# Kernel optimization log

Hardware: AMD Instinct MI355X
Metric: run time of the kernel (lower is better)

## Reference

```python
import jax, jax.numpy as jnp
import numpy as np

VOCAB_SIZE = 95
EMBED_DIM = 48
HIDDEN_DIM = 48


def setup_inputs() -> dict:
    key = jax.random.key(0)
    ks = jax.random.split(key, 8)
    B, S = 2048, 512
    x = jax.random.randint(ks[0], (B, S), 0, VOCAB_SIZE)
    s_e = 1.0  # torch Embedding default init ~ N(0,1); scale irrelevant for correctness
    emb = jax.random.normal(ks[1], (VOCAB_SIZE, EMBED_DIM), dtype=jnp.float32) * s_e
    k = 1.0 / np.sqrt(HIDDEN_DIM)
    w_ih = jax.random.uniform(ks[2], (3 * HIDDEN_DIM, EMBED_DIM), minval=-k, maxval=k, dtype=jnp.float32)
    w_hh = jax.random.uniform(ks[3], (3 * HIDDEN_DIM, HIDDEN_DIM), minval=-k, maxval=k, dtype=jnp.float32)
    b_ih = jax.random.uniform(ks[4], (3 * HIDDEN_DIM,), minval=-k, maxval=k, dtype=jnp.float32)
    b_hh = jax.random.uniform(ks[5], (3 * HIDDEN_DIM,), minval=-k, maxval=k, dtype=jnp.float32)
    w_out = jax.random.uniform(ks[6], (VOCAB_SIZE, HIDDEN_DIM), minval=-k, maxval=k, dtype=jnp.float32)
    b_out = jax.random.uniform(ks[7], (VOCAB_SIZE,), minval=-k, maxval=k, dtype=jnp.float32)
    return {"x": x, "emb": emb, "w_ih": w_ih, "w_hh": w_hh,
            "b_ih": b_ih, "b_hh": b_hh, "w_out": w_out, "b_out": b_out}


def _gru(embed, w_ih, w_hh, b_ih, b_hh):
    # embed: [B, S, E]. PyTorch GRU (single layer, batch_first):
    #   r = sig(Wir x + bir + Whr h + bhr); z = sig(Wiz x + biz + Whz h + bhz)
    B = embed.shape[0]
    H = w_hh.shape[1]
    # precompute input contributions for all timesteps: [S, B, 3H]
    xg = jnp.einsum('bse,ge->bsg', embed, w_ih) + b_ih
    xg = jnp.swapaxes(xg, 0, 1)
    h0 = jnp.zeros((B, H), dtype=embed.dtype)

    def step(h, xg_t):
        gh = h @ w_hh.T + b_hh  # [B, 3H]
        xr, xz, xn = jnp.split(xg_t, 3, axis=-1)
        hr, hz, hn = jnp.split(gh, 3, axis=-1)
        r = jax.nn.sigmoid(xr + hr)
        z = jax.nn.sigmoid(xz + hz)
        n = jnp.tanh(xn + r * hn)
        h_new = (1.0 - z) * n + z * h
        return h_new, h_new

    h_last, hs = jax.lax.scan(step, h0, xg)
    out = jnp.swapaxes(hs, 0, 1)  # [B, S, H]
    return out, h_last


def reference(x, emb, w_ih, w_hh, b_ih, b_hh, w_out, b_out):
    embed = emb[x]  # [B, S, E]
    out, h_last = _gru(embed, w_ih, w_hh, b_ih, b_hh)
    logits = jnp.einsum('bsh,vh->bsv', out, w_out) + b_out  # [B, S, V]
    hidden = h_last[None]  # [1, B, H] to match torch GRU hidden layout
    return logits, hidden
```

## Files before the change

### kernel.cpp

```cpp
#include <hip/hip_runtime.h>
#include <hip/hip_bf16.h>


#define BATCH 2048
#define SEQ   512
#define HDIM  48
#define VOCAB 95
#define G3    144

__device__ __forceinline__ float sigmoidf_(float x) {
    return 1.0f / (1.0f + __expf(-x));
}

__global__ void xg_precompute(const float* __restrict__ emb,
                              const float* __restrict__ w_ih,
                              const float* __restrict__ b_ih,
                              float* __restrict__ xg) {
    int v = blockIdx.x;
    int g = threadIdx.x;
    const float* e = emb + v * HDIM;
    const float* w = w_ih + g * HDIM;
    float a0 = 0.f, a1 = 0.f, a2 = 0.f, a3 = 0.f;
    #pragma unroll
    for (int k = 0; k < HDIM; k += 4) {
        a0 = fmaf(w[k + 0], e[k + 0], a0);
        a1 = fmaf(w[k + 1], e[k + 1], a1);
        a2 = fmaf(w[k + 2], e[k + 2], a2);
        a3 = fmaf(w[k + 3], e[k + 3], a3);
    }
    xg[v * G3 + g] = b_ih[g] + ((a0 + a1) + (a2 + a3));
}

__global__ __launch_bounds__(64, 2)
void gru_rec(const int* __restrict__ x,
             const float* __restrict__ xg_table,
             const float* __restrict__ w_hh,
             const float* __restrict__ b_hh,
             float* __restrict__ out,
             float* __restrict__ hidden) {
    const int row = blockIdx.x;
    const int j   = threadIdx.x;
    __shared__ float hsh[HDIM];

    float4 wr[12], wz[12], wn[12];
    float br = 0.f, bz = 0.f, bn = 0.f;
    float hj = 0.f;
    if (j < HDIM) {
        const float4* whr = (const float4*)(w_hh + (j         ) * HDIM);
        const float4* whz = (const float4*)(w_hh + (j +   HDIM) * HDIM);
        const float4* whn = (const float4*)(w_hh + (j + 2*HDIM) * HDIM);
        #pragma unroll
        for (int k = 0; k < 12; ++k) { wr[k] = whr[k]; wz[k] = whz[k]; wn[k] = whn[k]; }
        br = b_hh[j]; bz = b_hh[j + HDIM]; bn = b_hh[j + 2*HDIM];
        hsh[j] = 0.f;
    }
    __syncthreads();

    const int* xrow = x + row * SEQ;
    int tok = xrow[0];
    for (int t = 0; t < SEQ; ++t) {
        int tok_next = (t + 1 < SEQ) ? xrow[t + 1] : 0;
        float hnew = 0.f;
        if (j < HDIM) {
            const float* xg = xg_table + tok * G3;
            float xr = xg[j], xz = xg[j + HDIM], xn = xg[j + 2*HDIM];
            float accr = br, accz = bz, accn = bn;
            const float4* h4 = (const float4*)hsh;
            #pragma unroll
            for (int k = 0; k < 12; ++k) {
                float4 hh = h4[k];
                accr = fmaf(wr[k].x, hh.x, accr); accr = fmaf(wr[k].y, hh.y, accr);
                accr = fmaf(wr[k].z, hh.z, accr); accr = fmaf(wr[k].w, hh.w, accr);
                accz = fmaf(wz[k].x, hh.x, accz); accz = fmaf(wz[k].y, hh.y, accz);
                accz = fmaf(wz[k].z, hh.z, accz); accz = fmaf(wz[k].w, hh.w, accz);
                accn = fmaf(wn[k].x, hh.x, accn); accn = fmaf(wn[k].y, hh.y, accn);
                accn = fmaf(wn[k].z, hh.z, accn); accn = fmaf(wn[k].w, hh.w, accn);
            }
            float r = sigmoidf_(xr + accr);
            float z = sigmoidf_(xz + accz);
            float n = tanhf(xn + r * accn);
            hnew = (1.0f - z) * n + z * hj;
            hj = hnew;
            out[((long)(row * SEQ + t)) * VOCAB + j] = hnew;
        }
        __syncthreads();
        if (j < HDIM) hsh[j] = hnew;
        __syncthreads();
        tok = tok_next;
    }
    if (j < HDIM) hidden[row * HDIM + j] = hj;
}

__global__ __launch_bounds__(256, 2)
void logits_k(const float* __restrict__ w_out,
              const float* __restrict__ b_out,
              float* __restrict__ out) {
    __shared__ float hsh[256 * HDIM];
    const long pos0 = (long)blockIdx.x * 256;
    const int tid = threadIdx.x;

    for (int i = tid; i < 256 * HDIM; i += 256) {
        int p = i / HDIM;
        int k = i - p * HDIM;
        hsh[i] = out[(pos0 + p) * VOCAB + k];
    }
    __syncthreads();

    float h[HDIM];
    #pragma unroll
    for (int k = 0; k < 12; ++k)
        ((float4*)h)[k] = ((const float4*)(hsh + tid * HDIM))[k];

    float* orow = out + (pos0 + tid) * VOCAB;
    for (int v = 0; v < VOCAB; ++v) {
        const float* w = w_out + v * HDIM;
        float a0 = 0.f, a1 = 0.f, a2 = 0.f, a3 = 0.f;
        #pragma unroll
        for (int k = 0; k < HDIM; k += 4) {
            a0 = fmaf(w[k + 0], h[k + 0], a0);
            a1 = fmaf(w[k + 1], h[k + 1], a1);
            a2 = fmaf(w[k + 2], h[k + 2], a2);
            a3 = fmaf(w[k + 3], h[k + 3], a3);
        }
        orow[v] = b_out[v] + ((a0 + a1) + (a2 + a3));
    }
}

extern "C" void kernel_launch(void* const* d_in, const int* in_sizes, int n_in,
                              void* d_out, int out_size, void* d_ws, size_t ws_size,
                              hipStream_t stream) {
    const int*   x     = (const int*)d_in[0];
    const float* emb   = (const float*)d_in[1];
    const float* w_ih  = (const float*)d_in[2];
    const float* w_hh  = (const float*)d_in[3];
    const float* b_ih  = (const float*)d_in[4];
    const float* b_hh  = (const float*)d_in[5];
    const float* w_out = (const float*)d_in[6];
    const float* b_out = (const float*)d_in[7];

    float* out    = (float*)d_out;
    float* hidden = out + (long)BATCH * SEQ * VOCAB;
    float* xg     = (float*)d_ws;

    xg_precompute<<<VOCAB, G3, 0, stream>>>(emb, w_ih, b_ih, xg);
    gru_rec<<<BATCH, 64, 0, stream>>>(x, xg, w_hh, b_hh, out, hidden);
    logits_k<<<(BATCH * SEQ) / 256, 256, 0, stream>>>(w_out, b_out, out);
}
```

Measured before the change: 1.321 ms.

## Restructure logits kernel: split vocab across waves and stage output through LDS

The logits kernel now handles 64 positions per block, with each of the four waves computing a 24-wide slice of the vocabulary for the same 64 positions. Results go into shared memory and are then written back with coalesced float4 stores, replacing strided per-thread row writes of 95 floats. Hidden states are read with a padded stride of 49 to avoid LDS bank conflicts. This targets uncoalesced global stores in a kernel whose output dominates traffic, at the cost of extra LDS round trips and more blocks.

```diff
diff --git a/kernel.cpp b/kernel.cpp
--- a/kernel.cpp
+++ b/kernel.cpp
@@ -7,6 +7,7 @@
 #define HDIM  48
 #define VOCAB 95
 #define G3    144
+#define LPOS  64
 
 __device__ __forceinline__ float sigmoidf_(float x) {
     return 1.0f / (1.0f + __expf(-x));
@@ -91,28 +92,33 @@
     if (j < HDIM) hidden[row * HDIM + j] = hj;
 }
 
-__global__ __launch_bounds__(256, 2)
+__global__ __launch_bounds__(256, 4)
 void logits_k(const float* __restrict__ w_out,
               const float* __restrict__ b_out,
               float* __restrict__ out) {
-    __shared__ float hsh[256 * HDIM];
-    const long pos0 = (long)blockIdx.x * 256;
-    const int tid = threadIdx.x;
+    __shared__ __align__(16) float lsm[LPOS * VOCAB];
 
-    for (int i = tid; i < 256 * HDIM; i += 256) {
+    const long pos0 = (long)blockIdx.x * LPOS;
+    const int  tid  = threadIdx.x;
+    const int  lane = tid & 63;
+    const int  wv   = __builtin_amdgcn_readfirstlane(tid >> 6);
+
+    for (int i = tid; i < LPOS * HDIM; i += 256) {
         int p = i / HDIM;
         int k = i - p * HDIM;
-        hsh[i] = out[(pos0 + p) * VOCAB + k];
+        lsm[p * 49 + k] = out[(pos0 + p) * VOCAB + k];
     }
     __syncthreads();
 
+    const int p = lane;
     float h[HDIM];
     #pragma unroll
-    for (int k = 0; k < 12; ++k)
-        ((float4*)h)[k] = ((const float4*)(hsh + tid * HDIM))[k];
+    for (int k = 0; k < HDIM; ++k) h[k] = lsm[p * 49 + k];
+    __syncthreads();
 
-    float* orow = out + (pos0 + tid) * VOCAB;
-    for (int v = 0; v < VOCAB; ++v) {
+    const int v0 = wv * 24;
+    const int v1 = (v0 + 24 < VOCAB) ? (v0 + 24) : VOCAB;
+    for (int v = v0; v < v1; ++v) {
         const float* w = w_out + v * HDIM;
         float a0 = 0.f, a1 = 0.f, a2 = 0.f, a3 = 0.f;
         #pragma unroll
@@ -122,8 +128,14 @@
             a2 = fmaf(w[k + 2], h[k + 2], a2);
             a3 = fmaf(w[k + 3], h[k + 3], a3);
         }
-        orow[v] = b_out[v] + ((a0 + a1) + (a2 + a3));
+        lsm[p * VOCAB + v] = b_out[v] + ((a0 + a1) + (a2 + a3));
     }
+    __syncthreads();
+
+    float4*       dst = (float4*)(out + pos0 * VOCAB);
+    const float4* src = (const float4*)lsm;
+    for (int i = tid; i < (LPOS * VOCAB) / 4; i += 256)
+        dst[i] = src[i];
 }
 
 extern "C" void kernel_launch(void* const* d_in, const int* in_sizes, int n_in,
@@ -144,5 +156,5 @@
 
     xg_precompute<<<VOCAB, G3, 0, stream>>>(emb, w_ih, b_ih, xg);
     gru_rec<<<BATCH, 64, 0, stream>>>(x, xg, w_hh, b_hh, out, hidden);
-    logits_k<<<(BATCH * SEQ) / 256, 256, 0, stream>>>(w_out, b_out, out);
+    logits_k<<<(BATCH * SEQ) / LPOS, 256, 0, stream>>>(w_out, b_out, out);
 }
```

New measurement: 1.166 ms. 11.7% less time.

## Fuse GRU recurrence and output projection with producer/consumer warps

Applied to the files above, without the earlier changes.

Merges the recurrence and logits kernels into one launch. Wave 0 runs the GRU step and wave 1 computes the vocab projection from a double-buffered shared hidden state, so the hidden states no longer round-trip through global memory. The change also cuts to one barrier per step, prefetches the next token's input gates, pins weights in registers with asm, and replaces tanhf with an exp-based tanh. The risk is that per-step barrier coupling between the two waves may serialise the projection onto the critical path, and the fast tanh is less accurate.

```diff
diff --git a/kernel.cpp b/kernel.cpp
--- a/kernel.cpp
+++ b/kernel.cpp
@@ -1,5 +1,4 @@
 #include <hip/hip_runtime.h>
-#include <hip/hip_bf16.h>
 
 
 #define BATCH 2048
@@ -10,6 +9,9 @@
 
 __device__ __forceinline__ float sigmoidf_(float x) {
     return 1.0f / (1.0f + __expf(-x));
+}
+__device__ __forceinline__ float tanhf_(float x) {
+    return 1.0f - 2.0f / (__expf(2.0f * x) + 1.0f);
 }
 
 __global__ void xg_precompute(const float* __restrict__ emb,
@@ -31,41 +33,56 @@
     xg[v * G3 + g] = b_ih[g] + ((a0 + a1) + (a2 + a3));
 }
 
-__global__ __launch_bounds__(64, 2)
-void gru_rec(const int* __restrict__ x,
-             const float* __restrict__ xg_table,
-             const float* __restrict__ w_hh,
-             const float* __restrict__ b_hh,
-             float* __restrict__ out,
-             float* __restrict__ hidden) {
-    const int row = blockIdx.x;
-    const int j   = threadIdx.x;
-    __shared__ float hsh[HDIM];
+#define PIN4(f) asm volatile("" : "+v"((f).x), "+v"((f).y), "+v"((f).z), "+v"((f).w))
 
-    float4 wr[12], wz[12], wn[12];
-    float br = 0.f, bz = 0.f, bn = 0.f;
-    float hj = 0.f;
-    if (j < HDIM) {
-        const float4* whr = (const float4*)(w_hh + (j         ) * HDIM);
-        const float4* whz = (const float4*)(w_hh + (j +   HDIM) * HDIM);
-        const float4* whn = (const float4*)(w_hh + (j + 2*HDIM) * HDIM);
+__global__ __launch_bounds__(128, 2)
+void gru_fused(const int* __restrict__ x,
+               const float* __restrict__ xg_table,
+               const float* __restrict__ w_hh,
+               const float* __restrict__ b_hh,
+               const float* __restrict__ w_out,
+               const float* __restrict__ b_out,
+               float* __restrict__ out,
+               float* __restrict__ hidden) {
+    const int row  = blockIdx.x;
+    const int tid  = threadIdx.x;
+    const int lane = tid & 63;
+    const int wid  = __builtin_amdgcn_readfirstlane(tid >> 6);
+
+    __shared__ __align__(16) float hbuf[2][HDIM];
+
+    float* orow = out + (long)row * SEQ * VOCAB;
+
+    if (wid == 0) {
+        const int j  = lane;
+        const int jj = (j < HDIM) ? j : (j - HDIM);
+
+        float4 wr[12], wz[12], wn[12];
+        const float4* whr = (const float4*)(w_hh + (jj         ) * HDIM);
+        const float4* whz = (const float4*)(w_hh + (jj +   HDIM) * HDIM);
+        const float4* whn = (const float4*)(w_hh + (jj + 2*HDIM) * HDIM);
         #pragma unroll
         for (int k = 0; k < 12; ++k) { wr[k] = whr[k]; wz[k] = whz[k]; wn[k] = whn[k]; }
-        br = b_hh[j]; bz = b_hh[j + HDIM]; bn = b_hh[j + 2*HDIM];
-        hsh[j] = 0.f;
-    }
-    __syncthreads();
+        #pragma unroll
+        for (int k = 0; k < 12; ++k) { PIN4(wr[k]); PIN4(wz[k]); PIN4(wn[k]); }
+        float br = b_hh[jj], bz = b_hh[jj + HDIM], bn = b_hh[jj + 2*HDIM];
 
-    const int* xrow = x + row * SEQ;
-    int tok = xrow[0];
-    for (int t = 0; t < SEQ; ++t) {
-        int tok_next = (t + 1 < SEQ) ? xrow[t + 1] : 0;
-        float hnew = 0.f;
-        if (j < HDIM) {
-            const float* xg = xg_table + tok * G3;
-            float xr = xg[j], xz = xg[j + HDIM], xn = xg[j + 2*HDIM];
+        if (j < HDIM) hbuf[1][j] = 0.f;
+        float hj = 0.f;
+
+        const int* xrow = x + row * SEQ;
+        float xr, xz, xn;
+        {
+            const float* xg0 = xg_table + xrow[0] * G3;
+            xr = xg0[jj]; xz = xg0[jj + HDIM]; xn = xg0[jj + 2*HDIM];
+        }
+
+        for (int t = 0; t < SEQ; ++t) {
+            const float* xgn = xg_table + xrow[(t + 1 < SEQ) ? t + 1 : t] * G3;
+            float xrn = xgn[jj], xzn = xgn[jj + HDIM], xnn = xgn[jj + 2*HDIM];
+
+            const float4* h4 = (const float4*)hbuf[(t + 1) & 1];
             float accr = br, accz = bz, accn = bn;
-            const float4* h4 = (const float4*)hsh;
             #pragma unroll
             for (int k = 0; k < 12; ++k) {
                 float4 hh = h4[k];
@@ -78,51 +95,44 @@
             }
             float r = sigmoidf_(xr + accr);
             float z = sigmoidf_(xz + accz);
-            float n = tanhf(xn + r * accn);
-            hnew = (1.0f - z) * n + z * hj;
+            float n = tanhf_(xn + r * accn);
+            float hnew = (1.0f - z) * n + z * hj;
             hj = hnew;
-            out[((long)(row * SEQ + t)) * VOCAB + j] = hnew;
+            if (j < HDIM) hbuf[t & 1][j] = hnew;
+            __syncthreads();
+            xr = xrn; xz = xzn; xn = xnn;
         }
-        __syncthreads();
-        if (j < HDIM) hsh[j] = hnew;
-        __syncthreads();
-        tok = tok_next;
-    }
-    if (j < HDIM) hidden[row * HDIM + j] = hj;
-}
+        if (j < HDIM) hidden[row * HDIM + j] = hj;
+    } else {
+        const int v1 = lane;
+        const int v2 = (lane < VOCAB - 64) ? (lane + 64) : (VOCAB - 1);
+        const bool do2 = (lane < VOCAB - 64);
 
-__global__ __launch_bounds__(256, 2)
-void logits_k(const float* __restrict__ w_out,
-              const float* __restrict__ b_out,
-              float* __restrict__ out) {
-    __shared__ float hsh[256 * HDIM];
-    const long pos0 = (long)blockIdx.x * 256;
-    const int tid = threadIdx.x;
+        float4 wa[12], wb[12];
+        const float4* wva = (const float4*)(w_out + v1 * HDIM);
+        const float4* wvb = (const float4*)(w_out + v2 * HDIM);
+        #pragma unroll
+        for (int k = 0; k < 12; ++k) { wa[k] = wva[k]; wb[k] = wvb[k]; }
+        #pragma unroll
+        for (int k = 0; k < 12; ++k) { PIN4(wa[k]); PIN4(wb[k]); }
+        float ba = b_out[v1], bb = b_out[v2];
 
-    for (int i = tid; i < 256 * HDIM; i += 256) {
-        int p = i / HDIM;
-        int k = i - p * HDIM;
-        hsh[i] = out[(pos0 + p) * VOCAB + k];
-    }
-    __syncthreads();
-
-    float h[HDIM];
-    #pragma unroll
-    for (int k = 0; k < 12; ++k)
-        ((float4*)h)[k] = ((const float4*)(hsh + tid * HDIM))[k];
-
-    float* orow = out + (pos0 + tid) * VOCAB;
-    for (int v = 0; v < VOCAB; ++v) {
-        const float* w = w_out + v * HDIM;
-        float a0 = 0.f, a1 = 0.f, a2 = 0.f, a3 = 0.f;
-        #pragma unroll
-        for (int k = 0; k < HDIM; k += 4) {
-            a0 = fmaf(w[k + 0], h[k + 0], a0);
-            a1 = fmaf(w[k + 1], h[k + 1], a1);
-            a2 = fmaf(w[k + 2], h[k + 2], a2);
-            a3 = fmaf(w[k + 3], h[k + 3], a3);
+        for (int t = 0; t < SEQ; ++t) {
+            __syncthreads();
+            const float4* h4 = (const float4*)hbuf[t & 1];
+            float a0 = ba, b0 = bb;
+            #pragma unroll
+            for (int k = 0; k < 12; ++k) {
+                float4 hh = h4[k];
+                a0 = fmaf(wa[k].x, hh.x, a0); a0 = fmaf(wa[k].y, hh.y, a0);
+                a0 = fmaf(wa[k].z, hh.z, a0); a0 = fmaf(wa[k].w, hh.w, a0);
+                b0 = fmaf(wb[k].x, hh.x, b0); b0 = fmaf(wb[k].y, hh.y, b0);
+                b0 = fmaf(wb[k].z, hh.z, b0); b0 = fmaf(wb[k].w, hh.w, b0);
+            }
+            float* po = orow + (long)t * VOCAB;
+            po[v1] = a0;
+            if (do2) po[v2] = b0;
         }
-        orow[v] = b_out[v] + ((a0 + a1) + (a2 + a3));
     }
 }
 
@@ -143,6 +153,5 @@
     float* xg     = (float*)d_ws;
 
     xg_precompute<<<VOCAB, G3, 0, stream>>>(emb, w_ih, b_ih, xg);
-    gru_rec<<<BATCH, 64, 0, stream>>>(x, xg, w_hh, b_hh, out, hidden);
-    logits_k<<<(BATCH * SEQ) / 256, 256, 0, stream>>>(w_out, b_out, out);
+    gru_fused<<<BATCH, 128, 0, stream>>>(x, xg, w_hh, b_hh, w_out, b_out, out, hidden);
 }
```

Result: faster. 1.108 ms (-16.1%).
